# Optimization experiments

Measured on AMD Instinct MI355X. Metric: run time of the kernel, lower is better.

## Reference

```python
import jax, jax.numpy as jnp
import numpy as np
from jax import lax

B, CIN, COUT, K, SDIM, H = 8, 512, 512, 3, 512, 32
EPS = 1e-8
LRELU_SLOPE = 0.2
ACT_SCALE = float(np.sqrt(2.0))


def setup_inputs() -> dict:
    key = jax.random.key(0)
    k1, k2, k3, k4 = jax.random.split(key, 4)
    return {
        "x": jax.random.normal(k1, (B, CIN, H, H), jnp.float32),
        "style": jax.random.normal(k2, (B, SDIM), jnp.float32),
        "weight": jax.random.normal(k3, (COUT, CIN, K, K), jnp.float32),
        "mod_w": jax.random.normal(k4, (CIN, SDIM), jnp.float32),
        "mod_b": jnp.ones((CIN,), jnp.float32),  # EqualLinear bias_init=1
        "bias": jnp.zeros((COUT,), jnp.float32),  # FusedLeakyReLU bias
    }


def _blur_kernel(c):
    bk = np.array([1.0, 3.0, 3.0, 1.0], np.float32)
    bk = bk[None, :] * bk[:, None]
    bk = bk / bk.sum() * 4.0  # upsample_factor ** 2
    return jnp.tile(jnp.asarray(bk)[None, None], (c, 1, 1, 1))  # (C,1,4,4)


def reference(x, style, weight, mod_w, mod_b, bias):
    b, cin, h, w = x.shape
    cout, k = weight.shape[0], weight.shape[-1]
    conv_scale = 1.0 / np.sqrt(cin * k * k)
    lin_scale = 1.0 / np.sqrt(mod_w.shape[1])

    # style modulation: EqualLinear(style_dim -> in_channel), bias_init=1
    s = style @ (mod_w * lin_scale).T + mod_b  # (B, Cin)

    # per-sample modulated weights (B, Cout, Cin, k, k)
    wmod = conv_scale * weight[None] * s[:, None, :, None, None]
    demod = lax.rsqrt(jnp.sum(wmod * wmod, axis=(2, 3, 4)) + EPS)
    wmod = wmod * demod[:, :, None, None, None]

    # conv_transpose2d(stride=2, pad=0) == conv with lhs_dilation=2, pad=k-1,
    # spatially-flipped kernel (torch transposes (Cout,Cin)->(Cin,Cout)).
    wflip = jnp.flip(wmod, (-2, -1))

    def convt(xi, wi):  # xi: (Cin,H,W), wi: (Cout,Cin,k,k)
        return lax.conv_general_dilated(
            xi[None], wi, (1, 1), [(k - 1, k - 1)] * 2,
            lhs_dilation=(2, 2),
            dimension_numbers=("NCHW", "OIHW", "NCHW"))[0]

    y = jax.vmap(convt)(x, wflip)  # (B, Cout, 2H+1, 2W+1)

    # Blur: upfirdn2d with pad=(1,1), depthwise 4x4 FIR (kernel symmetric)
    bk = _blur_kernel(cout)
    y = lax.conv_general_dilated(
        y, bk, (1, 1), [(1, 1), (1, 1)],
        feature_group_count=cout,
        dimension_numbers=("NCHW", "OIHW", "NCHW"))  # (B, Cout, 2H, 2W)

    # FusedLeakyReLU: leaky_relu(y + bias) * sqrt(2)
    z = y + bias[None, :, None, None]
    return jnp.where(z >= 0, z, LRELU_SLOPE * z) * ACT_SCALE
```

## Files before the change

### kernel.cpp

```cpp
#include <hip/hip_runtime.h>
#include <hip/hip_bf16.h>

#define NB 8
#define CIN 512
#define COUT 512
#define SDIM 512

typedef __attribute__((ext_vector_type(8))) short short8;
typedef __attribute__((ext_vector_type(4))) float f32x4;

static constexpr float CONV_SCALE = 0.014731391274719740f;
static constexpr float LIN_SCALE  = 0.044194173824159216f;

static constexpr size_t OFF_S     = 0;
static constexpr size_t OFF_WSQ   = 16384;
static constexpr size_t OFF_DEMOD = 1064960;
static constexpr size_t OFF_XP    = 1081344;
static constexpr size_t OFF_WP    = 10551296;
static constexpr size_t OFF_Y1    = 15269888;
static constexpr size_t XP_BYTES  = 9469952;

static constexpr int NJOBS = 1060;

__device__ __forceinline__ int wpoff(int ps) {
  return ps == 0 ? 0 : ps == 1 ? 1048576 : ps == 2 ? 1572864 : 2097152;
}
__device__ __forceinline__ constexpr int y1off(int ps) {
  return ps == 0 ? 0 : ps == 1 ? 4460544 : ps == 2 ? 8785920 : 13111296;
}

__device__ __forceinline__ short f2bf(float f) {
  unsigned u = __builtin_bit_cast(unsigned, f);
  unsigned r = (u + 0x7fffu + ((u >> 16) & 1u)) >> 16;
  return (short)r;
}

__device__ __forceinline__ void load_lds16(const short* g, short* l) {
  __builtin_amdgcn_global_load_lds(
      (const __attribute__((address_space(1))) unsigned int*)g,
      (__attribute__((address_space(3))) unsigned int*)l, 16, 0, 0);
}

__global__ void k_style(const float* __restrict__ style, const float* __restrict__ mod_w,
                        const float* __restrict__ mod_b, float* __restrict__ s_out) {
  int wid = threadIdx.x >> 6, lane = threadIdx.x & 63;
  int ci = blockIdx.x * 4 + wid;
  float acc[NB] = {};
  for (int k = lane; k < SDIM; k += 64) {
    float wm = mod_w[ci * SDIM + k];
#pragma unroll
    for (int b = 0; b < NB; ++b) acc[b] += wm * style[b * SDIM + k];
  }
#pragma unroll
  for (int b = 0; b < NB; ++b) {
    float v = acc[b];
    for (int o = 32; o > 0; o >>= 1) v += __shfl_xor(v, o);
    if (lane == 0) s_out[b * CIN + ci] = v * LIN_SCALE + mod_b[ci];
  }
}

__global__ void k_wprep(const float* __restrict__ w, short* __restrict__ wp,
                        float* __restrict__ wsq) {
  int idx = blockIdx.x * blockDim.x + threadIdx.x;
  int co = idx >> 9, ci = idx & 511;
  float wv[3][3];
  float sq = 0.f;
#pragma unroll
  for (int i = 0; i < 9; ++i) {
    float v = w[idx * 9 + i];
    wv[i / 3][i % 3] = v;
    sq += v * v;
  }
  wsq[idx] = sq * CONV_SCALE * CONV_SCALE;
#pragma unroll
  for (int wy = 0; wy < 3; ++wy)
#pragma unroll
    for (int wx = 0; wx < 3; ++wx) {
      int psy = (wy == 1) ? 1 : 0, psx = (wx == 1) ? 1 : 0;
      int u = psy ? 0 : (wy == 0 ? 1 : 0);
      int v = psx ? 0 : (wx == 0 ? 1 : 0);
      int ps = psy * 2 + psx;
      int tap = psy ? (psx ? 0 : v) : (psx ? u : u * 2 + v);
      int k = tap * 512 + ci;
      int elem = wpoff(ps) + ((k >> 6) * 512 + co) * 64 + (k & 63);
      wp[elem] = f2bf(wv[wy][wx] * CONV_SCALE);
    }
}

__global__ void k_demod(const float* __restrict__ wsq, const float* __restrict__ s,
                        float* __restrict__ demod) {
  int wid = threadIdx.x >> 6, lane = threadIdx.x & 63;
  int co = blockIdx.x * 4 + wid;
  float acc[NB] = {};
  for (int ci = lane; ci < CIN; ci += 64) {
    float wq = wsq[co * CIN + ci];
#pragma unroll
    for (int b = 0; b < NB; ++b) {
      float sv = s[b * CIN + ci];
      acc[b] += wq * sv * sv;
    }
  }
#pragma unroll
  for (int b = 0; b < NB; ++b) {
    float v = acc[b];
    for (int o = 32; o > 0; o >>= 1) v += __shfl_xor(v, o);
    if (lane == 0) demod[b * COUT + co] = rsqrtf(v + 1e-8f);
  }
}

__global__ void k_xprep(const float* __restrict__ x, const float* __restrict__ s,
                        short* __restrict__ xp) {
  __shared__ float t[64][65];
  int sp0 = blockIdx.x * 64, ci0 = blockIdx.y * 64, b = blockIdx.z;
  for (int r = threadIdx.y; r < 64; r += 4)
    t[r][threadIdx.x] = x[(b * CIN + ci0 + r) * 1024 + sp0 + threadIdx.x];
  __syncthreads();
  int ci = ci0 + threadIdx.x;
  float sv = s[b * CIN + ci];
  for (int r = threadIdx.y; r < 64; r += 4) {
    int sp = sp0 + r;
    int yy = sp >> 5, xx = sp & 31;
    xp[((b * 34 + yy + 1) * 34 + (xx + 1)) * 512 + ci] = f2bf(t[threadIdx.x][r] * sv);
  }
}

#define MFMA_ROWPAIR(AH, AL, RH, RL)                                              \
  __builtin_amdgcn_s_setprio(1);                                                  \
  acc[RH][0] = __builtin_amdgcn_mfma_f32_16x16x32_bf16(AH, b0, acc[RH][0], 0,0,0);\
  acc[RH][1] = __builtin_amdgcn_mfma_f32_16x16x32_bf16(AH, b1, acc[RH][1], 0,0,0);\
  acc[RH][2] = __builtin_amdgcn_mfma_f32_16x16x32_bf16(AH, b2, acc[RH][2], 0,0,0);\
  acc[RH][3] = __builtin_amdgcn_mfma_f32_16x16x32_bf16(AH, b3, acc[RH][3], 0,0,0);\
  acc[RL][0] = __builtin_amdgcn_mfma_f32_16x16x32_bf16(AL, b0, acc[RL][0], 0,0,0);\
  acc[RL][1] = __builtin_amdgcn_mfma_f32_16x16x32_bf16(AL, b1, acc[RL][1], 0,0,0);\
  acc[RL][2] = __builtin_amdgcn_mfma_f32_16x16x32_bf16(AL, b2, acc[RL][2], 0,0,0);\
  acc[RL][3] = __builtin_amdgcn_mfma_f32_16x16x32_bf16(AL, b3, acc[RL][3], 0,0,0);\
  __builtin_amdgcn_s_setprio(0);

__global__ __launch_bounds__(256, 2) void k_gemm(const short* __restrict__ xp,
                                                 const short* __restrict__ wp,
                                                 float* __restrict__ y1) {
  __shared__ short sW[2][128 * 64];
  __shared__ short sX[2][128 * 64];

  const int tid = threadIdx.x;
  const int wid = tid >> 6, lane = tid & 63;
  const int hi = lane >> 4;
  const int ksw8 = ((tid & 7) ^ ((tid >> 3) & 7)) * 8;
  const int wm = (wid >> 1) * 64, wn = (wid & 1) * 64;

  const int bx = blockIdx.x;
  const int xcd = bx & 7, ii = bx >> 3;
  const int j = (((ii >> 2) << 3) + xcd) * 4 + (ii & 3);
  if (j >= NJOBS) return;

  int ps, base;
  if (j < 276)      { ps = 0; base = 0; }
  else if (j < 540) { ps = 1; base = 276; }
  else if (j < 804) { ps = 2; base = 540; }
  else              { ps = 3; base = 804; }
  const int r = j - base;
  const int nb = r >> 2, mb = r & 3;
  const int psy = ps >> 1, psx = ps & 1;
  const int Ny = 33 - psy, Nx = 33 - psx;
  const int N = NB * Ny * Nx;
  const int n0 = nb * 128, m0 = mb * 128;
  const int KT = (2 - psy) * (2 - psx) * 8;
  const short* wpb = wp + wpoff(ps);
  float* y1b = y1 + y1off(ps);

  int bb[4], ay[4], ax[4];
#pragma unroll
  for (int i = 0; i < 4; ++i) {
    int seg = i * 256 + tid;
    int n = n0 + (seg >> 3);
    if (n >= N) n = N - 1;
    int b = n / (Ny * Nx);
    int rem = n - b * (Ny * Nx);
    int a_y = rem / Nx;
    bb[i] = b; ay[i] = a_y; ax[i] = rem - a_y * Nx;
  }

  auto STAGE = [&](int kt, int d) {
    int tap = kt >> 3, ci0 = (kt & 7) << 6;
    int oy, ox;
    if (ps == 0)      { oy = tap >> 1; ox = tap & 1; }
    else if (ps == 1) { oy = tap;      ox = 1; }
    else if (ps == 2) { oy = 1;        ox = tap; }
    else              { oy = 1;        ox = 1; }
#pragma unroll
    for (int i = 0; i < 4; ++i) {
      int seg = i * 256 + tid;
      const short* gw = wpb + (kt * 512 + m0 + (seg >> 3)) * 64 + ksw8;
      load_lds16(gw, &sW[d][(i * 4 + wid) * 512]);
    }
#pragma unroll
    for (int i = 0; i < 4; ++i) {
      const short* gx = xp + ((bb[i] * 34 + ay[i] + oy) * 34 + ax[i] + ox) * 512 + ci0 + ksw8;
      load_lds16(gx, &sX[d][(i * 4 + wid) * 512]);
    }
  };

  const int c0 = ((hi)     ^ (lane & 7)) * 8;
  const int c1 = ((4 + hi) ^ (lane & 7)) * 8;
  const int rA0 = (wm +  0 + (lane & 15)) * 64, rA1 = (wm + 16 + (lane & 15)) * 64;
  const int rA2 = (wm + 32 + (lane & 15)) * 64, rA3 = (wm + 48 + (lane & 15)) * 64;
  const int rB0 = (wn +  0 + (lane & 15)) * 64, rB1 = (wn + 16 + (lane & 15)) * 64;
  const int rB2 = (wn + 32 + (lane & 15)) * 64, rB3 = (wn + 48 + (lane & 15)) * 64;

  f32x4 acc[4][4] = {};

  STAGE(0, 0);
  STAGE(1, 1);
  __syncthreads();

  int cur = 0;
  for (int t = 0; t < KT; ++t) {
    const short* W = sW[cur];
    const short* X = sX[cur];
    short8 a0, a1, b0, b1, b2, b3;

    a0 = *(const short8*)&W[rA0 + c0];
    a1 = *(const short8*)&W[rA1 + c0];
    b0 = *(const short8*)&X[rB0 + c0];
    b1 = *(const short8*)&X[rB1 + c0];
    b2 = *(const short8*)&X[rB2 + c0];
    b3 = *(const short8*)&X[rB3 + c0];
    MFMA_ROWPAIR(a0, a1, 0, 1);
    __builtin_amdgcn_s_barrier();

    a0 = *(const short8*)&W[rA2 + c0];
    a1 = *(const short8*)&W[rA3 + c0];
    MFMA_ROWPAIR(a0, a1, 2, 3);
    __builtin_amdgcn_s_barrier();

    a0 = *(const short8*)&W[rA0 + c1];
    a1 = *(const short8*)&W[rA1 + c1];
    b0 = *(const short8*)&X[rB0 + c1];
    b1 = *(const short8*)&X[rB1 + c1];
    b2 = *(const short8*)&X[rB2 + c1];
    b3 = *(const short8*)&X[rB3 + c1];
    MFMA_ROWPAIR(a0, a1, 0, 1);
    __builtin_amdgcn_s_barrier();

    a0 = *(const short8*)&W[rA2 + c1];
    a1 = *(const short8*)&W[rA3 + c1];
    MFMA_ROWPAIR(a0, a1, 2, 3);

    __syncthreads();
    if (t + 2 < KT) STAGE(t + 2, cur);
    cur ^= 1;
  }

#pragma unroll
  for (int mf = 0; mf < 4; ++mf) {
    int m = m0 + wm + mf * 16 + (lane >> 4) * 4;
#pragma unroll
    for (int nf = 0; nf < 4; ++nf) {
      int n = n0 + wn + nf * 16 + (lane & 15);
      if (n < N) {
#pragma unroll
        for (int rr = 0; rr < 4; ++rr) y1b[(m + rr) * N + n] = acc[mf][nf][rr];
      }
    }
  }
}

__global__ __launch_bounds__(256, 4) void k_blur(const float* __restrict__ y1,
                                                 const float* __restrict__ demod,
                                                 const float* __restrict__ bias,
                                                 float* __restrict__ out) {
  __shared__ float sin_[4][35 * 35];
  __shared__ float stmp[2][35][64];
  const int tid = threadIdx.x;
  const int bc = blockIdx.x;
  const int co = bc & 511, b = bc >> 9;

  for (int i = tid; i < 4 * 35 * 35; i += 256) ((float*)sin_)[i] = 0.f;
  __syncthreads();

#pragma unroll
  for (int ps = 0; ps < 4; ++ps) {
    const int Nyv = 33 - (ps >> 1), Nxv = 33 - (ps & 1);
    const float* pl = y1 + y1off(ps) + (co * NB + b) * (Nyv * Nxv);
    for (int t = tid; t < Nyv * Nxv; t += 256) {
      int av = t / Nxv, ah = t - av * Nxv;
      sin_[ps][(av + 1) * 35 + ah + 1] = pl[t];
    }
  }
  __syncthreads();

  const int q = tid & 63;
  const int mx = q >> 1, fx = q & 1;
  int xp0, xi0, xp1, xi1, xp2, xi2, xp3, xi3;
  if (fx) { xp0 = 0; xi0 = mx + 1; xp1 = 1; xi1 = mx + 1; xp2 = 0; xi2 = mx + 2; xp3 = 1; xi3 = mx + 2; }
  else    { xp0 = 1; xi0 = mx;     xp1 = 0; xi1 = mx + 1; xp2 = 1; xi2 = mx + 1; xp3 = 0; xi3 = mx + 2; }

  for (int r = tid >> 6; r < 70; r += 4) {
    int pv = (r >= 35) ? 1 : 0;
    int av = r - pv * 35;
    float v = 0.25f * sin_[pv * 2 + xp0][av * 35 + xi0]
            + 0.75f * sin_[pv * 2 + xp1][av * 35 + xi1]
            + 0.75f * sin_[pv * 2 + xp2][av * 35 + xi2]
            + 0.25f * sin_[pv * 2 + xp3][av * 35 + xi3];
    stmp[pv][av][q] = v;
  }
  __syncthreads();

  const float dm = demod[b * COUT + co], bs = bias[co];
  for (int p = tid >> 6; p < 64; p += 4) {
    int my = p >> 1, fy = p & 1;
    float v;
    if (fy) v = 0.25f * stmp[0][my + 1][q] + 0.75f * stmp[1][my + 1][q]
              + 0.75f * stmp[0][my + 2][q] + 0.25f * stmp[1][my + 2][q];
    else    v = 0.25f * stmp[1][my][q]     + 0.75f * stmp[0][my + 1][q]
              + 0.75f * stmp[1][my + 1][q] + 0.25f * stmp[0][my + 2][q];
    float val = dm * v + bs;
    out[(bc * 64 + p) * 64 + q] = (val >= 0.f ? val : 0.2f * val) * 1.41421356237309515f;
  }
}

extern "C" void kernel_launch(void* const* d_in, const int* in_sizes, int n_in,
                              void* d_out, int out_size, void* d_ws, size_t ws_size,
                              hipStream_t stream) {
  const float* x      = (const float*)d_in[0];
  const float* style  = (const float*)d_in[1];
  const float* weight = (const float*)d_in[2];
  const float* mod_w  = (const float*)d_in[3];
  const float* mod_b  = (const float*)d_in[4];
  const float* bias   = (const float*)d_in[5];
  float* out = (float*)d_out;
  char* ws = (char*)d_ws;

  float* s     = (float*)(ws + OFF_S);
  float* wsq   = (float*)(ws + OFF_WSQ);
  float* demod = (float*)(ws + OFF_DEMOD);
  short* xp    = (short*)(ws + OFF_XP);
  short* wp    = (short*)(ws + OFF_WP);
  float* y1    = (float*)(ws + OFF_Y1);

  hipMemsetAsync(xp, 0, XP_BYTES, stream);
  k_style<<<128, 256, 0, stream>>>(style, mod_w, mod_b, s);
  k_wprep<<<1024, 256, 0, stream>>>(weight, wp, wsq);
  k_demod<<<128, 256, 0, stream>>>(wsq, s, demod);
  k_xprep<<<dim3(16, 8, 8), dim3(64, 4), 0, stream>>>(x, s, xp);
  k_gemm<<<1088, 256, 0, stream>>>(xp, wp, y1);
  k_blur<<<4096, 256, 0, stream>>>(y1, demod, bias, out);
}
```

Measured before the change: 142.4 us.

## Store conv intermediate in bf16 and merge prep kernels into two launches

The GEMM now writes its intermediate result as bf16 instead of fp32, and the blur kernel reads bf16 and widens it to float. This halves the intermediate's write and read traffic at the cost of extra rounding before demodulation and blur. The four prep kernels (style, weight prep, demod, x prep) are also merged into two launches by branching on block index, which cuts launch overhead and lets independent work run side by side.

```diff
diff --git a/kernel.cpp b/kernel.cpp
--- a/kernel.cpp
+++ b/kernel.cpp
@@ -34,6 +34,9 @@
   unsigned r = (u + 0x7fffu + ((u >> 16) & 1u)) >> 16;
   return (short)r;
 }
+__device__ __forceinline__ float bf2f(unsigned short u) {
+  return __builtin_bit_cast(float, (unsigned)u << 16);
+}
 
 __device__ __forceinline__ void load_lds16(const short* g, short* l) {
   __builtin_amdgcn_global_load_lds(
@@ -41,86 +44,91 @@
       (__attribute__((address_space(3))) unsigned int*)l, 16, 0, 0);
 }
 
-__global__ void k_style(const float* __restrict__ style, const float* __restrict__ mod_w,
-                        const float* __restrict__ mod_b, float* __restrict__ s_out) {
-  int wid = threadIdx.x >> 6, lane = threadIdx.x & 63;
-  int ci = blockIdx.x * 4 + wid;
-  float acc[NB] = {};
-  for (int k = lane; k < SDIM; k += 64) {
-    float wm = mod_w[ci * SDIM + k];
-#pragma unroll
-    for (int b = 0; b < NB; ++b) acc[b] += wm * style[b * SDIM + k];
-  }
-#pragma unroll
-  for (int b = 0; b < NB; ++b) {
-    float v = acc[b];
-    for (int o = 32; o > 0; o >>= 1) v += __shfl_xor(v, o);
-    if (lane == 0) s_out[b * CIN + ci] = v * LIN_SCALE + mod_b[ci];
-  }
-}
-
-__global__ void k_wprep(const float* __restrict__ w, short* __restrict__ wp,
+__global__ void k_prep1(const float* __restrict__ style, const float* __restrict__ mod_w,
+                        const float* __restrict__ mod_b, float* __restrict__ s_out,
+                        const float* __restrict__ w, short* __restrict__ wp,
                         float* __restrict__ wsq) {
-  int idx = blockIdx.x * blockDim.x + threadIdx.x;
-  int co = idx >> 9, ci = idx & 511;
-  float wv[3][3];
-  float sq = 0.f;
-#pragma unroll
-  for (int i = 0; i < 9; ++i) {
-    float v = w[idx * 9 + i];
-    wv[i / 3][i % 3] = v;
-    sq += v * v;
-  }
-  wsq[idx] = sq * CONV_SCALE * CONV_SCALE;
-#pragma unroll
-  for (int wy = 0; wy < 3; ++wy)
-#pragma unroll
-    for (int wx = 0; wx < 3; ++wx) {
-      int psy = (wy == 1) ? 1 : 0, psx = (wx == 1) ? 1 : 0;
-      int u = psy ? 0 : (wy == 0 ? 1 : 0);
-      int v = psx ? 0 : (wx == 0 ? 1 : 0);
-      int ps = psy * 2 + psx;
-      int tap = psy ? (psx ? 0 : v) : (psx ? u : u * 2 + v);
-      int k = tap * 512 + ci;
-      int elem = wpoff(ps) + ((k >> 6) * 512 + co) * 64 + (k & 63);
-      wp[elem] = f2bf(wv[wy][wx] * CONV_SCALE);
-    }
-}
-
-__global__ void k_demod(const float* __restrict__ wsq, const float* __restrict__ s,
-                        float* __restrict__ demod) {
-  int wid = threadIdx.x >> 6, lane = threadIdx.x & 63;
-  int co = blockIdx.x * 4 + wid;
-  float acc[NB] = {};
-  for (int ci = lane; ci < CIN; ci += 64) {
-    float wq = wsq[co * CIN + ci];
+  const int tid = threadIdx.x;
+  if (blockIdx.x < 1024) {
+    int idx = blockIdx.x * 256 + tid;
+    int co = idx >> 9, ci = idx & 511;
+    float wv[3][3];
+    float sq = 0.f;
+#pragma unroll
+    for (int i = 0; i < 9; ++i) {
+      float v = w[idx * 9 + i];
+      wv[i / 3][i % 3] = v;
+      sq += v * v;
+    }
+    wsq[idx] = sq * CONV_SCALE * CONV_SCALE;
+#pragma unroll
+    for (int wy = 0; wy < 3; ++wy)
+#pragma unroll
+      for (int wx = 0; wx < 3; ++wx) {
+        int psy = (wy == 1) ? 1 : 0, psx = (wx == 1) ? 1 : 0;
+        int u = psy ? 0 : (wy == 0 ? 1 : 0);
+        int v = psx ? 0 : (wx == 0 ? 1 : 0);
+        int ps = psy * 2 + psx;
+        int tap = psy ? (psx ? 0 : v) : (psx ? u : u * 2 + v);
+        int k = tap * 512 + ci;
+        int elem = wpoff(ps) + ((k >> 6) * 512 + co) * 64 + (k & 63);
+        wp[elem] = f2bf(wv[wy][wx] * CONV_SCALE);
+      }
+  } else {
+    int wid = tid >> 6, lane = tid & 63;
+    int ci = (blockIdx.x - 1024) * 4 + wid;
+    float acc[NB] = {};
+    for (int k = lane; k < SDIM; k += 64) {
+      float wm = mod_w[ci * SDIM + k];
+#pragma unroll
+      for (int b = 0; b < NB; ++b) acc[b] += wm * style[b * SDIM + k];
+    }
 #pragma unroll
     for (int b = 0; b < NB; ++b) {
-      float sv = s[b * CIN + ci];
-      acc[b] += wq * sv * sv;
-    }
-  }
-#pragma unroll
-  for (int b = 0; b < NB; ++b) {
-    float v = acc[b];
-    for (int o = 32; o > 0; o >>= 1) v += __shfl_xor(v, o);
-    if (lane == 0) demod[b * COUT + co] = rsqrtf(v + 1e-8f);
-  }
-}
-
-__global__ void k_xprep(const float* __restrict__ x, const float* __restrict__ s,
-                        short* __restrict__ xp) {
-  __shared__ float t[64][65];
-  int sp0 = blockIdx.x * 64, ci0 = blockIdx.y * 64, b = blockIdx.z;
-  for (int r = threadIdx.y; r < 64; r += 4)
-    t[r][threadIdx.x] = x[(b * CIN + ci0 + r) * 1024 + sp0 + threadIdx.x];
-  __syncthreads();
-  int ci = ci0 + threadIdx.x;
-  float sv = s[b * CIN + ci];
-  for (int r = threadIdx.y; r < 64; r += 4) {
-    int sp = sp0 + r;
-    int yy = sp >> 5, xx = sp & 31;
-    xp[((b * 34 + yy + 1) * 34 + (xx + 1)) * 512 + ci] = f2bf(t[threadIdx.x][r] * sv);
+      float v = acc[b];
+      for (int o = 32; o > 0; o >>= 1) v += __shfl_xor(v, o);
+      if (lane == 0) s_out[b * CIN + ci] = v * LIN_SCALE + mod_b[ci];
+    }
+  }
+}
+
+__global__ void k_prep2(const float* __restrict__ wsq, const float* __restrict__ s,
+                        float* __restrict__ demod,
+                        const float* __restrict__ x, short* __restrict__ xp) {
+  const int tid = threadIdx.x;
+  if (blockIdx.x < 1024) {
+    __shared__ float t[64][65];
+    const int tx = tid & 63, ty = tid >> 6;
+    int bx = blockIdx.x;
+    int sp0 = (bx & 15) * 64, ci0 = ((bx >> 4) & 7) * 64, b = bx >> 7;
+    for (int r = ty; r < 64; r += 4)
+      t[r][tx] = x[(b * CIN + ci0 + r) * 1024 + sp0 + tx];
+    __syncthreads();
+    int ci = ci0 + tx;
+    float sv = s[b * CIN + ci];
+    for (int r = ty; r < 64; r += 4) {
+      int sp = sp0 + r;
+      int yy = sp >> 5, xx = sp & 31;
+      xp[((b * 34 + yy + 1) * 34 + (xx + 1)) * 512 + ci] = f2bf(t[tx][r] * sv);
+    }
+  } else {
+    int wid = tid >> 6, lane = tid & 63;
+    int co = (blockIdx.x - 1024) * 4 + wid;
+    float acc[NB] = {};
+    for (int ci = lane; ci < CIN; ci += 64) {
+      float wq = wsq[co * CIN + ci];
+#pragma unroll
+      for (int b = 0; b < NB; ++b) {
+        float sv = s[b * CIN + ci];
+        acc[b] += wq * sv * sv;
+      }
+    }
+#pragma unroll
+    for (int b = 0; b < NB; ++b) {
+      float v = acc[b];
+      for (int o = 32; o > 0; o >>= 1) v += __shfl_xor(v, o);
+      if (lane == 0) demod[b * COUT + co] = rsqrtf(v + 1e-8f);
+    }
   }
 }
 
@@ -138,7 +146,7 @@
 
 __global__ __launch_bounds__(256, 2) void k_gemm(const short* __restrict__ xp,
                                                  const short* __restrict__ wp,
-                                                 float* __restrict__ y1) {
+                                                 short* __restrict__ y1) {
   __shared__ short sW[2][128 * 64];
   __shared__ short sX[2][128 * 64];
 
@@ -166,7 +174,7 @@
   const int n0 = nb * 128, m0 = mb * 128;
   const int KT = (2 - psy) * (2 - psx) * 8;
   const short* wpb = wp + wpoff(ps);
-  float* y1b = y1 + y1off(ps);
+  short* y1b = y1 + y1off(ps);
 
   int bb[4], ay[4], ax[4];
 #pragma unroll
@@ -259,13 +267,13 @@
       int n = n0 + wn + nf * 16 + (lane & 15);
       if (n < N) {
 #pragma unroll
-        for (int rr = 0; rr < 4; ++rr) y1b[(m + rr) * N + n] = acc[mf][nf][rr];
+        for (int rr = 0; rr < 4; ++rr) y1b[(m + rr) * N + n] = f2bf(acc[mf][nf][rr]);
       }
     }
   }
 }
 
-__global__ __launch_bounds__(256, 4) void k_blur(const float* __restrict__ y1,
+__global__ __launch_bounds__(256, 4) void k_blur(const short* __restrict__ y1,
                                                  const float* __restrict__ demod,
                                                  const float* __restrict__ bias,
                                                  float* __restrict__ out) {
@@ -281,10 +289,10 @@
 #pragma unroll
   for (int ps = 0; ps < 4; ++ps) {
     const int Nyv = 33 - (ps >> 1), Nxv = 33 - (ps & 1);
-    const float* pl = y1 + y1off(ps) + (co * NB + b) * (Nyv * Nxv);
+    const short* pl = y1 + y1off(ps) + (co * NB + b) * (Nyv * Nxv);
     for (int t = tid; t < Nyv * Nxv; t += 256) {
       int av = t / Nxv, ah = t - av * Nxv;
-      sin_[ps][(av + 1) * 35 + ah + 1] = pl[t];
+      sin_[ps][(av + 1) * 35 + ah + 1] = bf2f((unsigned short)pl[t]);
     }
   }
   __syncthreads();
@@ -336,13 +344,11 @@
   float* demod = (float*)(ws + OFF_DEMOD);
   short* xp    = (short*)(ws + OFF_XP);
   short* wp    = (short*)(ws + OFF_WP);
-  float* y1    = (float*)(ws + OFF_Y1);
+  short* y1    = (short*)(ws + OFF_Y1);
 
   hipMemsetAsync(xp, 0, XP_BYTES, stream);
-  k_style<<<128, 256, 0, stream>>>(style, mod_w, mod_b, s);
-  k_wprep<<<1024, 256, 0, stream>>>(weight, wp, wsq);
-  k_demod<<<128, 256, 0, stream>>>(wsq, s, demod);
-  k_xprep<<<dim3(16, 8, 8), dim3(64, 4), 0, stream>>>(x, s, xp);
+  k_prep1<<<1152, 256, 0, stream>>>(style, mod_w, mod_b, s, weight, wp, wsq);
+  k_prep2<<<1152, 256, 0, stream>>>(wsq, s, demod, x, xp);
   k_gemm<<<1088, 256, 0, stream>>>(xp, wp, y1);
   k_blur<<<4096, 256, 0, stream>>>(y1, demod, bias, out);
 }
```

Result: faster. 131.9 us (-7.3%).
